# Optimization experiments

Measured on AMD Instinct MI355X. Metric: run time of the kernel, lower is better.

The kernel has to match this reference:

```python
import jax, jax.numpy as jnp
import numpy as np

B, L, H, Di, N, K, R = 2, 512, 2048, 4096, 16, 4, 128


def setup_inputs() -> dict:
    key = jax.random.key(0)
    ks = jax.random.split(key, 8)
    s = 0.02
    inp = {
        "x": jax.random.normal(ks[0], (B, L, H), jnp.float32),
        "in_w": jax.random.normal(ks[1], (2 * Di, H), jnp.float32) * s,
        "in_b": jnp.zeros((2 * Di,), jnp.float32),
        "conv_w": jax.random.normal(ks[2], (Di, 1, K), jnp.float32) * s,  # depthwise conv weight
        "conv_b": jnp.zeros((Di,), jnp.float32),
        "xproj_w": jax.random.normal(ks[3], (R + 2 * N, Di), jnp.float32) * s,
        "dt_w": jax.random.normal(ks[4], (Di, R), jnp.float32) * s,
        "dt_b": jax.random.normal(ks[5], (Di,), jnp.float32) * 0.1,
        "A_log": jnp.log(jnp.broadcast_to(jnp.arange(1, N + 1, dtype=jnp.float32)[None, :], (Di, N))) + jnp.zeros((Di, N), jnp.float32),
        "D": jnp.ones((Di,), jnp.float32),
        "out_w": jax.random.normal(ks[6], (H, Di), jnp.float32) * s,
        "out_b": jnp.zeros((H,), jnp.float32),
    }
    return inp


def reference(x, in_w, in_b, conv_w, conv_b, xproj_w, dt_w, dt_b, A_log, D, out_w, out_b):
    silu = jax.nn.silu
    # in_proj -> split into hidden path and gate
    proj = x @ in_w.T + in_b                       # [B, L, 2*Di]
    h, gate = jnp.split(proj, 2, axis=-1)          # each [B, L, Di]
    # causal depthwise conv1d over time
    hc = jnp.transpose(h, (0, 2, 1))               # [B, Di, L]
    hc = jax.lax.conv_general_dilated(
        hc, conv_w, window_strides=(1,), padding=[(K - 1, 0)],
        dimension_numbers=("NCH", "OIH", "NCH"), feature_group_count=Di)
    hc = silu(hc + conv_b[None, :, None])          # [B, Di, L]
    hs = jnp.transpose(hc, (0, 2, 1))              # [B, L, Di]
    # input-dependent SSM parameters
    sp = hs @ xproj_w.T                            # [B, L, R + 2N]
    ts, Bm, Cm = sp[..., :R], sp[..., R:R + N], sp[..., R + N:]
    dt = jax.nn.softplus(ts @ dt_w.T + dt_b)       # [B, L, Di]
    A = -jnp.exp(A_log)                            # [Di, N]
    dA = jnp.exp(dt[..., None] * A[None, None])    # [B, L, Di, N]
    dBu = dt[..., None] * Bm[:, :, None, :] * hs[..., None]  # [B, L, Di, N]

    # selective scan: s_t = dA_t * s_{t-1} + dBu_t ; y_t = s_t . C_t
    def step(s, inputs):
        dA_t, dBu_t, C_t = inputs                  # [B,Di,N], [B,Di,N], [B,N]
        s = dA_t * s + dBu_t
        y = jnp.einsum("bdn,bn->bd", s, C_t)
        return s, y

    s0 = jnp.zeros((x.shape[0], Di, N), x.dtype)
    _, ys = jax.lax.scan(step, s0, (jnp.swapaxes(dA, 0, 1), jnp.swapaxes(dBu, 0, 1), jnp.swapaxes(Cm, 0, 1)))
    y = jnp.transpose(ys, (1, 0, 2))               # [B, L, Di]
    y = (y + hs * D) * silu(gate)
    return y @ out_w.T + out_b                     # [B, L, H]
```

## Files before the change

kernel.cpp:

```cpp
#include <hip/hip_runtime.h>
#include <hip/hip_bf16.h>

typedef __hip_bfloat16 bf16;
typedef short bf16x8 __attribute__((ext_vector_type(8)));
typedef float f32x4 __attribute__((ext_vector_type(4)));

#define BB 2
#define LL 512
#define HH 2048
#define DI 4096
#define NST 16
#define KK 4
#define RR 128
#define BLM (BB*LL)
#define CN 16
#define LC (LL/CN)
#define ZXP 16
#define ZOUT 4

enum { MODE_PROJ = 0, MODE_XPROJ = 1, MODE_DT = 2, MODE_OUT = 3 };

__device__ __forceinline__ float sigmoidf_(float x) { return 1.f / (1.f + __expf(-x)); }
__device__ __forceinline__ float softplusf_(float x) {
    return fmaxf(x, 0.f) + log1pf(__expf(-fabsf(x)));
}
__device__ __forceinline__ unsigned int bfpack(float a, float b) {
    __hip_bfloat162 h = __float22bfloat162_rn(make_float2(a, b));
    union { __hip_bfloat162 h; unsigned int u; } cv; cv.h = h;
    return cv.u;
}

typedef const __attribute__((address_space(1))) unsigned int* gas_t;
typedef __attribute__((address_space(3))) unsigned int* las_t;
__device__ __forceinline__ void gld16(const void* g, void* l) {
    __builtin_amdgcn_global_load_lds((gas_t)g, (las_t)l, 16, 0, 0);
}

__device__ __forceinline__ void cvt_seg(const float* s, bf16* d, int i) {
    float4 v = ((const float4*)s)[i];
    uint2 o; o.x = bfpack(v.x, v.y); o.y = bfpack(v.z, v.w);
    ((uint2*)d)[i] = o;
}

__global__ __launch_bounds__(256) void cvt_all(
    const float* __restrict__ s0, bf16* __restrict__ d0, int n0,
    const float* __restrict__ s1, bf16* __restrict__ d1, int n1,
    const float* __restrict__ s2, bf16* __restrict__ d2, int n2,
    const float* __restrict__ s3, bf16* __restrict__ d3, int n3)
{
    int i = blockIdx.x * 256 + threadIdx.x;
    int stride = gridDim.x * 256;
    int t1 = n0 + n1, t2 = t1 + n2, t3 = t2 + n3;
    for (; i < t3; i += stride) {
        if      (i < n0) cvt_seg(s0, d0, i);
        else if (i < t1) cvt_seg(s1, d1, i - n0);
        else if (i < t2) cvt_seg(s2, d2, i - t1);
        else             cvt_seg(s3, d3, i - t2);
    }
}

__global__ __launch_bounds__(256) void cvt_f32_bf16(
    const float* __restrict__ src, bf16* __restrict__ dst, int n4)
{
    int i = blockIdx.x * 256 + threadIdx.x;
    int stride = gridDim.x * 256;
    for (; i < n4; i += stride) cvt_seg(src, dst, i);
}

template<int BM, int MODE>
__global__ __launch_bounds__(256) void gemm_bf16(
    const bf16* __restrict__ A, const bf16* __restrict__ Bw,
    int N, int K, int lda, int ldb,
    const float* __restrict__ bias,
    float* __restrict__ outf, bf16* __restrict__ outh, bf16* __restrict__ outh2,
    float* __restrict__ s0, float* __restrict__ s1,
    float* __restrict__ s2, float* __restrict__ s3)
{
    __shared__ short sA[BM * 32];
    __shared__ short sB[128 * 32];
    const int tid = threadIdx.x;
    const int col0 = blockIdx.x * 128;
    const int row0 = blockIdx.y * BM;
    const int wave = tid >> 6;
    const int lane = tid & 63;
    constexpr int NJ = (BM == 128) ? 4 : 2;
    const int wr = (BM == 128) ? ((wave >> 1) * 64) : 0;
    const int wc = (BM == 128) ? ((wave & 1) * 64) : (wave * 32);
    const int lr = lane & 15;
    const int kq = (lane >> 4) << 3;

    const int kpb = K / gridDim.z;
    const int kbeg = blockIdx.z * kpb;
    const int kend = kbeg + kpb;

    const int r0 = tid >> 2;
    const int kc = (tid & 3) << 3;

    f32x4 acc[4][NJ] = {};

    for (int k0 = kbeg; k0 < kend; k0 += 32) {
        #pragma unroll
        for (int p = 0; p < BM / 64; p++) {
            int r = r0 + p * 64;
            gld16(A + (size_t)(row0 + r) * lda + k0 + kc, &sA[r * 32 + kc]);
        }
        #pragma unroll
        for (int p = 0; p < 2; p++) {
            int rr = r0 + p * 64;
            int nb = col0 + rr; if (nb > N - 1) nb = N - 1;
            gld16(Bw + (size_t)nb * ldb + k0 + kc, &sB[rr * 32 + kc]);
        }
        __syncthreads();
        bf16x8 af[4], bfr[NJ];
        #pragma unroll
        for (int i = 0; i < 4; i++)
            af[i] = *(const bf16x8*)(&sA[(wr + i * 16 + lr) * 32 + kq]);
        #pragma unroll
        for (int j = 0; j < NJ; j++)
            bfr[j] = *(const bf16x8*)(&sB[(wc + j * 16 + lr) * 32 + kq]);
        #pragma unroll
        for (int i = 0; i < 4; i++)
            #pragma unroll
            for (int j = 0; j < NJ; j++)
                acc[i][j] = __builtin_amdgcn_mfma_f32_16x16x32_bf16(af[i], bfr[j], acc[i][j], 0, 0, 0);
        __syncthreads();
    }

    float* oslice = outf;
    if (MODE == MODE_OUT) {
        int z = blockIdx.z;
        oslice = (z == 0) ? s0 : (z == 1) ? s1 : (z == 2) ? s2 : s3;
    }
    const int drow = (lane >> 4) << 2;
    const int dcol = lane & 15;
    #pragma unroll
    for (int i = 0; i < 4; i++) {
        #pragma unroll
        for (int j = 0; j < NJ; j++) {
            int n = col0 + wc + j * 16 + dcol;
            if (n >= N) continue;
            float bv = bias ? bias[n] : 0.f;
            #pragma unroll
            for (int r = 0; r < 4; r++) {
                int m = row0 + wr + i * 16 + drow + r;
                float v = acc[i][j][r];
                if (MODE == MODE_PROJ) {
                    v += bv;
                    if (n < DI) outh2[(size_t)m * DI + n] = (bf16)v;
                    else        outh[(size_t)m * DI + (n - DI)] = (bf16)v;
                } else if (MODE == MODE_XPROJ) {
                    outf[(size_t)blockIdx.z * (BLM * 160) + (size_t)m * 160 + n] = v;
                } else if (MODE == MODE_DT) {
                    outf[(size_t)m * DI + n] = softplusf_(v + bv);
                } else {
                    oslice[(size_t)m * HH + n] = v;
                }
            }
        }
    }
}

__global__ __launch_bounds__(256) void reduce_sp(
    const float* __restrict__ spS, float* __restrict__ sp_f, bf16* __restrict__ ts_b)
{
    int i = blockIdx.x * 256 + threadIdx.x;
    int row = i / 40, c4 = (i % 40) * 4;
    float4 s = make_float4(0.f, 0.f, 0.f, 0.f);
    #pragma unroll
    for (int z = 0; z < ZXP; z++) {
        float4 v = *(const float4*)&spS[(size_t)z * (BLM * 160) + (size_t)row * 160 + c4];
        s.x += v.x; s.y += v.y; s.z += v.z; s.w += v.w;
    }
    *(float4*)&sp_f[(size_t)row * 160 + c4] = s;
    if (c4 < RR) {
        uint2 o; o.x = bfpack(s.x, s.y); o.y = bfpack(s.z, s.w);
        *(uint2*)&ts_b[(size_t)row * RR + c4] = o;
    }
}

__global__ __launch_bounds__(256) void reduce_out(
    const float* __restrict__ s0, const float* __restrict__ s1,
    const float* __restrict__ s2, const float* __restrict__ s3,
    const float* __restrict__ bias, float* __restrict__ out)
{
    int i = blockIdx.x * 256 + threadIdx.x;
    int c4 = (i & 511) << 2;
    float4 a = ((const float4*)s0)[i];
    float4 b = ((const float4*)s1)[i];
    float4 c = ((const float4*)s2)[i];
    float4 d = ((const float4*)s3)[i];
    float4 bv = *(const float4*)&bias[c4];
    float4 r;
    r.x = a.x + b.x + c.x + d.x + bv.x;
    r.y = a.y + b.y + c.y + d.y + bv.y;
    r.z = a.z + b.z + c.z + d.z + bv.z;
    r.w = a.w + b.w + c.w + d.w + bv.w;
    ((float4*)out)[i] = r;
}

__global__ __launch_bounds__(256) void conv_silu(
    const bf16* __restrict__ h, const float* __restrict__ conv_w,
    const float* __restrict__ conv_b, bf16* __restrict__ hs_b)
{
    int idx = blockIdx.x * 256 + threadIdx.x;
    int d = idx & (DI - 1);
    int l = (idx >> 12) & (LL - 1);
    float acc = conv_b[d];
    #pragma unroll
    for (int k = 0; k < KK; k++) {
        int ls = l - (KK - 1) + k;
        if (ls >= 0) acc += (float)h[(size_t)idx + (size_t)(ls - l) * DI] * conv_w[d * KK + k];
    }
    float s = acc * sigmoidf_(acc);
    hs_b[idx] = (bf16)s;
}

__global__ __launch_bounds__(256) void scan_part1(
    const float* __restrict__ dtr, const float* __restrict__ sp,
    const bf16* __restrict__ hs_b, const float* __restrict__ A_log,
    float* __restrict__ P_ws, float* __restrict__ S_ws)
{
    int bid = blockIdx.x;
    int c  = bid & (CN - 1);
    int db = (bid >> 4) & (DI / 256 - 1);
    int b  = bid >> 8;
    int d  = db * 256 + threadIdx.x;

    float A[NST], P[NST], S[NST];
    #pragma unroll
    for (int n = 0; n < NST; n++) {
        A[n] = -__expf(A_log[d * NST + n]);
        P[n] = 1.f; S[n] = 0.f;
    }
    const float* spb = sp + (size_t)b * LL * 160;
    size_t base = (size_t)b * LL * DI + d;
    for (int l = c * LC; l < (c + 1) * LC; l++) {
        size_t off = base + (size_t)l * DI;
        float dtv = dtr[off];
        float hsv = (float)hs_b[off];
        float dh = dtv * hsv;
        #pragma unroll
        for (int n = 0; n < NST; n++) {
            float a  = __expf(dtv * A[n]);
            float Bn = spb[l * 160 + RR + n];
            S[n] = a * S[n] + dh * Bn;
            P[n] *= a;
        }
    }
    size_t o = ((size_t)((b * CN + c) * DI) + d) * NST;
    #pragma unroll
    for (int q = 0; q < 4; q++) {
        *(float4*)&P_ws[o + q * 4] = make_float4(P[q*4], P[q*4+1], P[q*4+2], P[q*4+3]);
        *(float4*)&S_ws[o + q * 4] = make_float4(S[q*4], S[q*4+1], S[q*4+2], S[q*4+3]);
    }
}

__global__ __launch_bounds__(256) void scan_part2(
    const float* __restrict__ dtr, const float* __restrict__ sp,
    const bf16* __restrict__ hs_b, const bf16* __restrict__ g_b,
    const float* __restrict__ A_log, const float* __restrict__ Dv,
    const float* __restrict__ P_ws, const float* __restrict__ S_ws,
    bf16* __restrict__ y_b)
{
    int bid = blockIdx.x;
    int c  = bid & (CN - 1);
    int db = (bid >> 4) & (DI / 256 - 1);
    int b  = bid >> 8;
    int d  = db * 256 + threadIdx.x;

    float s[NST];
    #pragma unroll
    for (int n = 0; n < NST; n++) s[n] = 0.f;
    for (int j = 0; j < c; j++) {
        size_t o = ((size_t)((b * CN + j) * DI) + d) * NST;
        #pragma unroll
        for (int q = 0; q < 4; q++) {
            float4 Pq = *(const float4*)&P_ws[o + q * 4];
            float4 Sq = *(const float4*)&S_ws[o + q * 4];
            s[q*4+0] = Pq.x * s[q*4+0] + Sq.x;
            s[q*4+1] = Pq.y * s[q*4+1] + Sq.y;
            s[q*4+2] = Pq.z * s[q*4+2] + Sq.z;
            s[q*4+3] = Pq.w * s[q*4+3] + Sq.w;
        }
    }

    float A[NST];
    #pragma unroll
    for (int n = 0; n < NST; n++) A[n] = -__expf(A_log[d * NST + n]);
    float Dd = Dv[d];

    const float* spb = sp + (size_t)b * LL * 160;
    size_t base = (size_t)b * LL * DI + d;
    for (int l = c * LC; l < (c + 1) * LC; l++) {
        size_t off = base + (size_t)l * DI;
        float dtv = dtr[off];
        float hsv = (float)hs_b[off];
        float dh = dtv * hsv;
        float y = 0.f;
        #pragma unroll
        for (int n = 0; n < NST; n++) {
            float a  = __expf(dtv * A[n]);
            float Bn = spb[l * 160 + RR + n];
            float Cn = spb[l * 160 + RR + NST + n];
            s[n] = a * s[n] + dh * Bn;
            y += s[n] * Cn;
        }
        float gv = (float)g_b[off];
        y_b[off] = (bf16)((y + hsv * Dd) * (gv * sigmoidf_(gv)));
    }
}

extern "C" void kernel_launch(void* const* d_in, const int* in_sizes, int n_in,
                              void* d_out, int out_size, void* d_ws, size_t ws_size,
                              hipStream_t stream)
{
    const float* x       = (const float*)d_in[0];
    const float* in_w    = (const float*)d_in[1];
    const float* in_b    = (const float*)d_in[2];
    const float* conv_w  = (const float*)d_in[3];
    const float* conv_b  = (const float*)d_in[4];
    const float* xproj_w = (const float*)d_in[5];
    const float* dt_w    = (const float*)d_in[6];
    const float* dt_b    = (const float*)d_in[7];
    const float* A_log   = (const float*)d_in[8];
    const float* Dv      = (const float*)d_in[9];
    const float* out_w   = (const float*)d_in[10];
    const float* out_b   = (const float*)d_in[11];
    float* out = (float*)d_out;

    char* ws = (char*)d_ws;
    const size_t MB = 1u << 20;
    bf16*  x_b    = (bf16*)(ws);
    float* spS    = (float*)(ws);
    float* P_ws   = (float*)(ws);
    float* S_ws   = (float*)(ws + 8 * MB);
    float* oS1    = (float*)(ws);
    bf16*  in_w_b = (bf16*)(ws + 16 * MB);
    bf16*  y_b    = (bf16*)(ws + 16 * MB);
    bf16*  hs_b   = (bf16*)(ws + 24 * MB);
    float* oS0    = (float*)(ws + 24 * MB);
    float* dt_f   = (float*)(ws + 32 * MB);
    bf16*  ow_b   = (bf16*)(ws + 32 * MB);
    bf16*  h_b    = (bf16*)(ws + 48 * MB);
    float* oS2    = (float*)(ws + 48 * MB);
    bf16*  g_b    = (bf16*)(ws + 56 * MB);
    float* oS3    = (float*)(ws + 56 * MB);
    char* p = ws + 64 * MB;
    float* sp_f = (float*)p; p += (size_t)BLM * 160 * 4;
    bf16*  ts_b = (bf16*)p;  p += (size_t)BLM * RR * 2;
    bf16*  xw_b = (bf16*)p;  p += (size_t)(RR + 2 * NST) * DI * 2;
    bf16*  dtw_b= (bf16*)p;  p += (size_t)DI * RR * 2;

    cvt_all<<<2048, 256, 0, stream>>>(
        x, x_b, BLM * HH / 4,
        in_w, in_w_b, 2 * DI * HH / 4,
        xproj_w, xw_b, (RR + 2 * NST) * DI / 4,
        dt_w, dtw_b, DI * RR / 4);
    gemm_bf16<128, MODE_PROJ><<<dim3((2 * DI) / 128, BLM / 128, 1), 256, 0, stream>>>(
        x_b, in_w_b, 2 * DI, HH, HH, HH, in_b, nullptr, g_b, h_b,
        nullptr, nullptr, nullptr, nullptr);
    conv_silu<<<(BLM * DI) / 256, 256, 0, stream>>>(h_b, conv_w, conv_b, hs_b);
    gemm_bf16<64, MODE_XPROJ><<<dim3(2, BLM / 64, ZXP), 256, 0, stream>>>(
        hs_b, xw_b, RR + 2 * NST, DI, DI, DI, nullptr, spS, nullptr, nullptr,
        nullptr, nullptr, nullptr, nullptr);
    reduce_sp<<<160, 256, 0, stream>>>(spS, sp_f, ts_b);
    gemm_bf16<64, MODE_DT><<<dim3(DI / 128, BLM / 64, 1), 256, 0, stream>>>(
        ts_b, dtw_b, DI, RR, RR, RR, dt_b, dt_f, nullptr, nullptr,
        nullptr, nullptr, nullptr, nullptr);
    scan_part1<<<BB * (DI / 256) * CN, 256, 0, stream>>>(
        dt_f, sp_f, hs_b, A_log, P_ws, S_ws);
    scan_part2<<<BB * (DI / 256) * CN, 256, 0, stream>>>(
        dt_f, sp_f, hs_b, g_b, A_log, Dv, P_ws, S_ws, y_b);
    cvt_f32_bf16<<<512, 256, 0, stream>>>(out_w, ow_b, HH * DI / 4);
    gemm_bf16<128, MODE_OUT><<<dim3(HH / 128, BLM / 128, ZOUT), 256, 0, stream>>>(
        y_b, ow_b, HH, DI, DI, DI, nullptr, nullptr, nullptr, nullptr,
        oS0, oS1, oS2, oS3);
    reduce_out<<<2048, 256, 0, stream>>>(oS0, oS1, oS2, oS3, out_b, out);
}
```

Baseline: 375.1 us.

## Use 128x64 GEMM tiles for in/out projections and fp16 split-K partials

Adds a BN template parameter so the input and output projection GEMMs use 128x64 tiles. This doubles the block count for more parallelism across CUs, at the cost of less B-tile reuse per block. The split-K partial sums for the output projection are now stored in fp16 instead of fp32, halving the partial-sum write and read traffic in the reduce step. The trade-off is lower precision in the partials and a workspace layout rearranged to fit the smaller buffers.

```diff
diff --git a/kernel.cpp b/kernel.cpp
--- a/kernel.cpp
+++ b/kernel.cpp
@@ -2,8 +2,10 @@
 #include <hip/hip_bf16.h>
 
 typedef __hip_bfloat16 bf16;
+typedef _Float16 fp16;
 typedef short bf16x8 __attribute__((ext_vector_type(8)));
 typedef float f32x4 __attribute__((ext_vector_type(4)));
+typedef _Float16 half8 __attribute__((ext_vector_type(8)));
 
 #define BB 2
 #define LL 512
@@ -67,25 +69,25 @@
     for (; i < n4; i += stride) cvt_seg(src, dst, i);
 }
 
-template<int BM, int MODE>
+template<int BM, int BN, int MODE>
 __global__ __launch_bounds__(256) void gemm_bf16(
     const bf16* __restrict__ A, const bf16* __restrict__ Bw,
     int N, int K, int lda, int ldb,
     const float* __restrict__ bias,
     float* __restrict__ outf, bf16* __restrict__ outh, bf16* __restrict__ outh2,
-    float* __restrict__ s0, float* __restrict__ s1,
-    float* __restrict__ s2, float* __restrict__ s3)
+    fp16* __restrict__ s0, fp16* __restrict__ s1,
+    fp16* __restrict__ s2, fp16* __restrict__ s3)
 {
     __shared__ short sA[BM * 32];
-    __shared__ short sB[128 * 32];
+    __shared__ short sB[BN * 32];
     const int tid = threadIdx.x;
-    const int col0 = blockIdx.x * 128;
+    const int col0 = blockIdx.x * BN;
     const int row0 = blockIdx.y * BM;
     const int wave = tid >> 6;
     const int lane = tid & 63;
-    constexpr int NJ = (BM == 128) ? 4 : 2;
+    constexpr int NJ = (BM == 64 || BN == 64) ? 2 : 4;
     const int wr = (BM == 128) ? ((wave >> 1) * 64) : 0;
-    const int wc = (BM == 128) ? ((wave & 1) * 64) : (wave * 32);
+    const int wc = (BM == 64) ? (wave * 32) : ((wave & 1) * (BN / 2));
     const int lr = lane & 15;
     const int kq = (lane >> 4) << 3;
 
@@ -105,7 +107,7 @@
             gld16(A + (size_t)(row0 + r) * lda + k0 + kc, &sA[r * 32 + kc]);
         }
         #pragma unroll
-        for (int p = 0; p < 2; p++) {
+        for (int p = 0; p < BN / 64; p++) {
             int rr = r0 + p * 64;
             int nb = col0 + rr; if (nb > N - 1) nb = N - 1;
             gld16(Bw + (size_t)nb * ldb + k0 + kc, &sB[rr * 32 + kc]);
@@ -126,7 +128,7 @@
         __syncthreads();
     }
 
-    float* oslice = outf;
+    fp16* oslice = nullptr;
     if (MODE == MODE_OUT) {
         int z = blockIdx.z;
         oslice = (z == 0) ? s0 : (z == 1) ? s1 : (z == 2) ? s2 : s3;
@@ -153,7 +155,7 @@
                 } else if (MODE == MODE_DT) {
                     outf[(size_t)m * DI + n] = softplusf_(v + bv);
                 } else {
-                    oslice[(size_t)m * HH + n] = v;
+                    oslice[(size_t)m * HH + n] = (fp16)v;
                 }
             }
         }
@@ -179,23 +181,22 @@
 }
 
 __global__ __launch_bounds__(256) void reduce_out(
-    const float* __restrict__ s0, const float* __restrict__ s1,
-    const float* __restrict__ s2, const float* __restrict__ s3,
+    const fp16* __restrict__ s0, const fp16* __restrict__ s1,
+    const fp16* __restrict__ s2, const fp16* __restrict__ s3,
     const float* __restrict__ bias, float* __restrict__ out)
 {
     int i = blockIdx.x * 256 + threadIdx.x;
-    int c4 = (i & 511) << 2;
-    float4 a = ((const float4*)s0)[i];
-    float4 b = ((const float4*)s1)[i];
-    float4 c = ((const float4*)s2)[i];
-    float4 d = ((const float4*)s3)[i];
-    float4 bv = *(const float4*)&bias[c4];
-    float4 r;
-    r.x = a.x + b.x + c.x + d.x + bv.x;
-    r.y = a.y + b.y + c.y + d.y + bv.y;
-    r.z = a.z + b.z + c.z + d.z + bv.z;
-    r.w = a.w + b.w + c.w + d.w + bv.w;
-    ((float4*)out)[i] = r;
+    int c8 = (i & 255) << 3;
+    half8 a = ((const half8*)s0)[i];
+    half8 b = ((const half8*)s1)[i];
+    half8 c = ((const half8*)s2)[i];
+    half8 d = ((const half8*)s3)[i];
+    float r[8];
+    #pragma unroll
+    for (int e = 0; e < 8; e++)
+        r[e] = (float)a[e] + (float)b[e] + (float)c[e] + (float)d[e] + bias[c8 + e];
+    ((float4*)out)[2 * i]     = make_float4(r[0], r[1], r[2], r[3]);
+    ((float4*)out)[2 * i + 1] = make_float4(r[4], r[5], r[6], r[7]);
 }
 
 __global__ __launch_bounds__(256) void conv_silu(
@@ -334,17 +335,17 @@
     float* spS    = (float*)(ws);
     float* P_ws   = (float*)(ws);
     float* S_ws   = (float*)(ws + 8 * MB);
-    float* oS1    = (float*)(ws);
+    fp16*  oS2    = (fp16*)(ws);
+    fp16*  oS3    = (fp16*)(ws + 4 * MB);
     bf16*  in_w_b = (bf16*)(ws + 16 * MB);
     bf16*  y_b    = (bf16*)(ws + 16 * MB);
     bf16*  hs_b   = (bf16*)(ws + 24 * MB);
-    float* oS0    = (float*)(ws + 24 * MB);
+    fp16*  oS0    = (fp16*)(ws + 24 * MB);
+    fp16*  oS1    = (fp16*)(ws + 28 * MB);
     float* dt_f   = (float*)(ws + 32 * MB);
     bf16*  ow_b   = (bf16*)(ws + 32 * MB);
     bf16*  h_b    = (bf16*)(ws + 48 * MB);
-    float* oS2    = (float*)(ws + 48 * MB);
     bf16*  g_b    = (bf16*)(ws + 56 * MB);
-    float* oS3    = (float*)(ws + 56 * MB);
     char* p = ws + 64 * MB;
     float* sp_f = (float*)p; p += (size_t)BLM * 160 * 4;
     bf16*  ts_b = (bf16*)p;  p += (size_t)BLM * RR * 2;
@@ -356,15 +357,15 @@
         in_w, in_w_b, 2 * DI * HH / 4,
         xproj_w, xw_b, (RR + 2 * NST) * DI / 4,
         dt_w, dtw_b, DI * RR / 4);
-    gemm_bf16<128, MODE_PROJ><<<dim3((2 * DI) / 128, BLM / 128, 1), 256, 0, stream>>>(
+    gemm_bf16<128, 64, MODE_PROJ><<<dim3((2 * DI) / 64, BLM / 128, 1), 256, 0, stream>>>(
         x_b, in_w_b, 2 * DI, HH, HH, HH, in_b, nullptr, g_b, h_b,
         nullptr, nullptr, nullptr, nullptr);
     conv_silu<<<(BLM * DI) / 256, 256, 0, stream>>>(h_b, conv_w, conv_b, hs_b);
-    gemm_bf16<64, MODE_XPROJ><<<dim3(2, BLM / 64, ZXP), 256, 0, stream>>>(
+    gemm_bf16<64, 128, MODE_XPROJ><<<dim3(2, BLM / 64, ZXP), 256, 0, stream>>>(
         hs_b, xw_b, RR + 2 * NST, DI, DI, DI, nullptr, spS, nullptr, nullptr,
         nullptr, nullptr, nullptr, nullptr);
     reduce_sp<<<160, 256, 0, stream>>>(spS, sp_f, ts_b);
-    gemm_bf16<64, MODE_DT><<<dim3(DI / 128, BLM / 64, 1), 256, 0, stream>>>(
+    gemm_bf16<64, 128, MODE_DT><<<dim3(DI / 128, BLM / 64, 1), 256, 0, stream>>>(
         ts_b, dtw_b, DI, RR, RR, RR, dt_b, dt_f, nullptr, nullptr,
         nullptr, nullptr, nullptr, nullptr);
     scan_part1<<<BB * (DI / 256) * CN, 256, 0, stream>>>(
@@ -372,8 +373,8 @@
     scan_part2<<<BB * (DI / 256) * CN, 256, 0, stream>>>(
         dt_f, sp_f, hs_b, g_b, A_log, Dv, P_ws, S_ws, y_b);
     cvt_f32_bf16<<<512, 256, 0, stream>>>(out_w, ow_b, HH * DI / 4);
-    gemm_bf16<128, MODE_OUT><<<dim3(HH / 128, BLM / 128, ZOUT), 256, 0, stream>>>(
+    gemm_bf16<128, 64, MODE_OUT><<<dim3(HH / 64, BLM / 128, ZOUT), 256, 0, stream>>>(
         y_b, ow_b, HH, DI, DI, DI, nullptr, nullptr, nullptr, nullptr,
         oS0, oS1, oS2, oS3);
-    reduce_out<<<2048, 256, 0, stream>>>(oS0, oS1, oS2, oS3, out_b, out);
-}
+    reduce_out<<<1024, 256, 0, stream>>>(oS0, oS1, oS2, oS3, out_b, out);
+}
```

New measurement: 368.3 us. Within noise of the previous version (-1.8%).
